# Kernel tuning notes

Hardware: AMD Instinct MI355X
Metric: run time of the kernel (lower is better)

The kernel has to match this reference:

```python
import jax, jax.numpy as jnp
import numpy as np

SIZE_DICT = 1024
DIM_DICT = 256
BETA = 0.001


def setup_inputs() -> dict:
    key = jax.random.key(0)
    k1, k2 = jax.random.split(key)
    z = jax.random.normal(k1, (64, 1024, DIM_DICT), dtype=jnp.float32)
    codebook = jax.random.normal(k2, (SIZE_DICT, DIM_DICT), dtype=jnp.float32)
    return {"z": z, "codebook": codebook, "flg_train": 1}


def reference(z, codebook, flg_train):
    zf = z.reshape(-1, DIM_DICT)  # [N, D]
    # squared euclidean distances: ||z||^2 + ||c||^2 - 2 z c^T  -> [N, K]
    d = (jnp.sum(zf ** 2, axis=1, keepdims=True)
         + jnp.sum(codebook ** 2, axis=1)
         - 2.0 * jnp.matmul(zf, codebook.T))
    idx = jnp.argmin(d, axis=1)  # [N]
    # one-hot @ codebook == gather
    z_q = codebook[idx].reshape(z.shape)
    if flg_train:
        loss = (jnp.mean((jax.lax.stop_gradient(z_q) - z) ** 2)
                + BETA * jnp.mean((z_q - jax.lax.stop_gradient(z)) ** 2))
    else:
        loss = jnp.float32(0.0)
    # straight-through estimator
    z_q = z + jax.lax.stop_gradient(z_q - z)
    # perplexity from codebook usage histogram (== mean of one-hot rows)
    n = zf.shape[0]
    counts = jax.ops.segment_sum(jnp.ones((n,), jnp.float32), idx,
                                 num_segments=SIZE_DICT)
    e_mean = counts / n
    perplexity = jnp.exp(-jnp.sum(e_mean * jnp.log(e_mean + 1e-10)))
    return (z_q, loss, perplexity)
```

## Files before the change

### kernel.cpp

```cpp
#include <hip/hip_runtime.h>


#define N_ROWS 65536
#define DIM    256
#define K_CODES 1024
#define BETA   0.001f

#define BM      128
#define NBLOCKS (N_ROWS / BM)
#define NTHREADS 512
#define CHUNK_BYTES 65536
#define NCHUNK  16

#define LO_SCALE 2048.0f
#define LO_INV   (1.0f / 2048.0f)

#define WS_BESTS_OFF 16384
#define WS_CBIMG_OFF 278528
#define WS_NEED (WS_CBIMG_OFF + NCHUNK * CHUNK_BYTES)

typedef _Float16 f16x8 __attribute__((ext_vector_type(8)));
typedef float f32x16 __attribute__((ext_vector_type(16)));


__global__ void cnorm_kernel(const float* __restrict__ cb, float* __restrict__ cnorm) {
    int k = blockIdx.x * blockDim.x + threadIdx.x;
    if (k >= K_CODES) return;
    const float4* row = (const float4*)(cb + (size_t)k * DIM);
    float s = 0.f;
#pragma unroll
    for (int j = 0; j < DIM / 4; ++j) {
        float4 v = row[j];
        s = fmaf(v.x, v.x, s);
        s = fmaf(v.y, v.y, s);
        s = fmaf(v.z, v.z, s);
        s = fmaf(v.w, v.w, s);
    }
    cnorm[k] = s;
}

__global__ void cb_prep(const float* __restrict__ cb, char* __restrict__ img) {
    int idx = blockIdx.x * blockDim.x + threadIdx.x;
    int c   = idx >> 5;
    int g32 = idx & 31;
    const float4* src = (const float4*)(cb + (size_t)c * DIM + g32 * 8);
    float4 v0 = src[0], v1 = src[1];
    float vv[8] = {v0.x, v0.y, v0.z, v0.w, v1.x, v1.y, v1.z, v1.w};
    f16x8 hi, lo;
#pragma unroll
    for (int j = 0; j < 8; ++j) {
        _Float16 h = (_Float16)vv[j];
        hi[j] = h;
        lo[j] = (_Float16)((vv[j] - (float)h) * LO_SCALE);
    }
    int kh = g32 >> 4;
    int gl = g32 & 15;
    int cl = c & 63;
    int unit = (c >> 6) * 2 + kh;
    size_t off = (size_t)unit * 32768 + (size_t)gl * 1024 + (size_t)cl * 16;
    *(f16x8*)(img + off) = hi;
    *(f16x8*)(img + off + 16384) = lo;
}


__device__ inline void stage_chunk(const char* img, int c, char* ldsbase, int tid) {
#pragma unroll
    for (int i = 0; i < 8; ++i) {
        __builtin_amdgcn_global_load_lds(
            (const __attribute__((address_space(1))) unsigned int*)
                (img + (size_t)c * CHUNK_BYTES + i * 8192 + tid * 16),
            (__attribute__((address_space(3))) unsigned int*)
                (ldsbase + i * 8192 + tid * 16),
            16, 0, 0);
    }
}

#define COMPUTE_CHUNK(BUF)                                                           \
    {                                                                                \
        const _Float16* bbase = csb + (BUF) * 32768 + crow * 8;                      \
        _Pragma("unroll")                                                            \
        for (int ks = 0; ks < 16; ++ks) {                                            \
            const _Float16* p = bbase + (ks >> 3) * 16384 + ((ks & 7) * 2 + lh) * 512;\
            f16x8 bh = *(const f16x8*)(p);                                           \
            f16x8 bl = *(const f16x8*)(p + 8192);                                    \
            f16x8 ah = zh[ks], al = zl[ks];                                          \
            acc_hh = __builtin_amdgcn_mfma_f32_32x32x16_f16(ah, bh, acc_hh, 0, 0, 0);\
            acc_x1 = __builtin_amdgcn_mfma_f32_32x32x16_f16(ah, bl, acc_x1, 0, 0, 0);\
            acc_x2 = __builtin_amdgcn_mfma_f32_32x32x16_f16(al, bh, acc_x2, 0, 0, 0);\
        }                                                                            \
    }

__global__ __launch_bounds__(NTHREADS, 2)
void vq_main_mfma(const float* __restrict__ z, const char* __restrict__ img,
                  const float* __restrict__ cnorm, int* __restrict__ bests_g,
                  int* __restrict__ counts, float* __restrict__ ploss) {
    __shared__ _Float16 csb[2 * 32768];
    __shared__ float bs2[BM][2];
    __shared__ int   bc2[BM][2];
    __shared__ float znorm_lds[BM];
    __shared__ float red[NTHREADS];

    const int tid  = threadIdx.x;
    const int lane = tid & 63;
    const int w    = tid >> 6;
    const int wr   = w >> 1;
    const int wc   = w & 1;
    const int l31  = lane & 31;
    const int lh   = lane >> 5;
    const int r0   = blockIdx.x * BM;

    stage_chunk(img, 0, (char*)csb, tid);

    const int zrow = wr * 32 + l31;
    f16x8 zh[16], zl[16];
    {
        const float* zr = z + (size_t)(r0 + zrow) * DIM;
        float zn = 0.f;
#pragma unroll
        for (int gi = 0; gi < 16; ++gi) {
            int g = gi * 2 + lh;
            float4 v0 = *(const float4*)(zr + g * 8);
            float4 v1 = *(const float4*)(zr + g * 8 + 4);
            float vv[8] = {v0.x, v0.y, v0.z, v0.w, v1.x, v1.y, v1.z, v1.w};
            f16x8 hi, lo;
#pragma unroll
            for (int j = 0; j < 8; ++j) {
                _Float16 h = (_Float16)vv[j];
                hi[j] = h;
                lo[j] = (_Float16)((vv[j] - (float)h) * LO_SCALE);
                zn = fmaf(vv[j], vv[j], zn);
            }
            zh[gi] = hi;
            zl[gi] = lo;
        }
        zn += __shfl_xor(zn, 32, 64);
        if (wc == 0 && lh == 0) znorm_lds[zrow] = zn;
    }

    f32x16 acc_hh, acc_x1, acc_x2;
#pragma unroll
    for (int e = 0; e < 16; ++e) { acc_hh[e] = 0.f; acc_x1[e] = 0.f; acc_x2[e] = 0.f; }
    float best_s[16];
    int   best_c[16];
#pragma unroll
    for (int e = 0; e < 16; ++e) { best_s[e] = 3.4e38f; best_c[e] = 0; }

    const int crow = wc * 32 + l31;

#pragma unroll 1
    for (int c = 0; c < NCHUNK; ++c) {
        const int b = c & 1;
        asm volatile("" ::: "memory");
        __builtin_amdgcn_s_barrier();
        asm volatile("" ::: "memory");
        if (c + 1 < NCHUNK) {
            stage_chunk(img, c + 1, (char*)csb + (b ^ 1) * CHUNK_BYTES, tid);
            asm volatile("s_waitcnt vmcnt(8)" ::: "memory");
        } else {
            asm volatile("s_waitcnt vmcnt(0)" ::: "memory");
        }
        __builtin_amdgcn_s_barrier();
        asm volatile("" ::: "memory");

        __builtin_amdgcn_s_setprio(1);
        COMPUTE_CHUNK(b)
        __builtin_amdgcn_s_setprio(0);

        {
            int col = c * 64 + crow;
            float cn = cnorm[col];
#pragma unroll
            for (int rg = 0; rg < 16; ++rg) {
                float dot = fmaf(acc_x1[rg] + acc_x2[rg], LO_INV, acc_hh[rg]);
                float s = fmaf(-2.0f, dot, cn);
                bool take = s < best_s[rg];
                best_s[rg] = take ? s : best_s[rg];
                best_c[rg] = take ? col : best_c[rg];
            }
#pragma unroll
            for (int e = 0; e < 16; ++e) { acc_hh[e] = 0.f; acc_x1[e] = 0.f; acc_x2[e] = 0.f; }
        }
    }

#pragma unroll
    for (int rg = 0; rg < 16; ++rg) {
        float bsv = best_s[rg];
        int   bcv = best_c[rg];
#pragma unroll
        for (int s = 1; s < 32; s <<= 1) {
            float os = __shfl_xor(bsv, s, 64);
            int   oc = __shfl_xor(bcv, s, 64);
            bool take = (os < bsv) || (os == bsv && oc < bcv);
            bsv = take ? os : bsv;
            bcv = take ? oc : bcv;
        }
        best_s[rg] = bsv;
        best_c[rg] = bcv;
    }
    if (l31 == 0) {
#pragma unroll
        for (int rg = 0; rg < 16; ++rg) {
            int rl = (rg & 3) + 8 * (rg >> 2) + 4 * lh;
            bs2[wr * 32 + rl][wc] = best_s[rg];
            bc2[wr * 32 + rl][wc] = best_c[rg];
        }
    }
    __syncthreads();

    float lsum = 0.f;
    if (tid < BM) {
        float s0 = bs2[tid][0], s1 = bs2[tid][1];
        int   c0 = bc2[tid][0], c1 = bc2[tid][1];
        bool t1 = (s1 < s0) || (s1 == s0 && c1 < c0);
        int   bc = t1 ? c1 : c0;
        float bs = t1 ? s1 : s0;
        bests_g[r0 + tid] = bc;
        atomicAdd(&counts[bc], 1);
        lsum = bs + znorm_lds[tid];
    }
    red[tid] = lsum;
    __syncthreads();
    for (int s = NTHREADS / 2; s > 0; s >>= 1) {
        if (tid < s) red[tid] += red[tid + s];
        __syncthreads();
    }
    if (tid == 0) ploss[blockIdx.x] = red[0];
}


__global__ __launch_bounds__(256)
void vq_gather(const float4* __restrict__ cb4, const int* __restrict__ bests,
               float4* __restrict__ out4) {
    int gid = blockIdx.x * blockDim.x + threadIdx.x;
    int row = gid >> 6;
    int q   = gid & 63;
    out4[gid] = cb4[(size_t)bests[row] * 64 + q];
}


#define FBM     32
#define FCHUNK  512
#define FDSTAGE 16
#define FCS_PAD 20
#define FNBLOCKS (N_ROWS / FBM)

__global__ __launch_bounds__(256, 2)
void vq_main_fp32(const float* __restrict__ z, const float* __restrict__ cb,
                  const float* __restrict__ cnorm, float* __restrict__ out,
                  int* __restrict__ counts, float* __restrict__ ploss) {
    __shared__ float zs[FBM][DIM];
    __shared__ float cs[FCHUNK][FCS_PAD];
    __shared__ int   bests[FBM];
    __shared__ float red[256];

    const int tid = threadIdx.x;
    const int tx  = tid & 63;
    const int ty  = tid >> 6;
    const int r0  = blockIdx.x * FBM;

    {
        const float4* zg  = (const float4*)(z + (size_t)r0 * DIM);
        float4*       zsv = (float4*)&zs[0][0];
#pragma unroll
        for (int j = 0; j < (FBM * DIM / 4) / 256; ++j)
            zsv[tid + 256 * j] = zg[tid + 256 * j];
    }

    unsigned long long best[8];
#pragma unroll
    for (int i = 0; i < 8; ++i) best[i] = ~0ull;

    for (int cb0 = 0; cb0 < K_CODES; cb0 += FCHUNK) {
        float acc[8][8];
#pragma unroll
        for (int i = 0; i < 8; ++i)
#pragma unroll
            for (int m = 0; m < 8; ++m) acc[i][m] = 0.f;

        for (int sd = 0; sd < DIM / FDSTAGE; ++sd) {
            __syncthreads();
#pragma unroll
            for (int j = 0; j < 8; ++j) {
                int f4i = tid + 256 * j;
                int c   = f4i >> 2;
                int qq  = f4i & 3;
                float4 v = *(const float4*)(cb + (size_t)(cb0 + c) * DIM + sd * FDSTAGE + qq * 4);
                *(float4*)&cs[c][qq * 4] = v;
            }
            __syncthreads();

#pragma unroll
            for (int dd4 = 0; dd4 < FDSTAGE / 4; ++dd4) {
                float4 zv[8], cv[8];
#pragma unroll
                for (int i = 0; i < 8; ++i)
                    zv[i] = *(const float4*)&zs[ty * 8 + i][sd * FDSTAGE + dd4 * 4];
#pragma unroll
                for (int m = 0; m < 8; ++m)
                    cv[m] = *(const float4*)&cs[tx + 64 * m][dd4 * 4];
#pragma unroll
                for (int i = 0; i < 8; ++i)
#pragma unroll
                    for (int m = 0; m < 8; ++m) {
                        float a = acc[i][m];
                        a = fmaf(zv[i].x, cv[m].x, a);
                        a = fmaf(zv[i].y, cv[m].y, a);
                        a = fmaf(zv[i].z, cv[m].z, a);
                        a = fmaf(zv[i].w, cv[m].w, a);
                        acc[i][m] = a;
                    }
            }
        }

#pragma unroll
        for (int m = 0; m < 8; ++m) {
            int   c  = cb0 + tx + 64 * m;
            float cn = cnorm[c];
#pragma unroll
            for (int i = 0; i < 8; ++i) {
                float s = fmaf(-2.f, acc[i][m], cn);
                unsigned u = __float_as_uint(s);
                u = (u & 0x80000000u) ? ~u : (u | 0x80000000u);
                unsigned long long key = ((unsigned long long)u << 32) | (unsigned)c;
                best[i] = key < best[i] ? key : best[i];
            }
        }
    }

#pragma unroll
    for (int i = 0; i < 8; ++i) {
        unsigned long long b = best[i];
#pragma unroll
        for (int s = 1; s < 64; s <<= 1) {
            unsigned long long o = __shfl_xor(b, s, 64);
            b = o < b ? o : b;
        }
        best[i] = b;
    }
    if (tx == 0)
#pragma unroll
        for (int i = 0; i < 8; ++i)
            bests[ty * 8 + i] = (int)(best[i] & 0xFFFFFFFFu);
    __syncthreads();

    const int r  = tid >> 3;
    const int lq = tid & 7;
    const int bidx = bests[r];
    const float4* crow = (const float4*)(cb + (size_t)bidx * DIM);
    const float4* zrow = (const float4*)&zs[r][0];
    float4*       orow = (float4*)(out + (size_t)(r0 + r) * DIM);
    float lsum = 0.f;
#pragma unroll
    for (int j = 0; j < 8; ++j) {
        int qg = lq + j * 8;
        float4 c4 = crow[qg];
        float4 z4 = zrow[qg];
        float4 o;
        float dx = c4.x - z4.x; o.x = z4.x + dx; lsum = fmaf(dx, dx, lsum);
        float dy = c4.y - z4.y; o.y = z4.y + dy; lsum = fmaf(dy, dy, lsum);
        float dz = c4.z - z4.z; o.z = z4.z + dz; lsum = fmaf(dz, dz, lsum);
        float dw = c4.w - z4.w; o.w = z4.w + dw; lsum = fmaf(dw, dw, lsum);
        orow[qg] = o;
    }
    if (tid < FBM) atomicAdd(&counts[bests[tid]], 1);

    red[tid] = lsum;
    __syncthreads();
    for (int s = 128; s > 0; s >>= 1) {
        if (tid < s) red[tid] += red[tid + s];
        __syncthreads();
    }
    if (tid == 0) ploss[blockIdx.x] = red[0];
}


__global__ void vq_final(const float* __restrict__ ploss, const int* __restrict__ counts,
                         const int* __restrict__ flg, float* __restrict__ out2, int np) {
    __shared__ float red[1024];
    const int t = threadIdx.x;

    float l = 0.f;
    for (int i = t; i < np; i += 1024) l += ploss[i];
    red[t] = l;
    __syncthreads();
    for (int s = 512; s > 0; s >>= 1) {
        if (t < s) red[t] += red[t + s];
        __syncthreads();
    }
    if (t == 0) {
        float loss = (red[0] / (float)((size_t)N_ROWS * DIM)) * (1.0f + BETA);
        if (flg[0] == 0) loss = 0.f;
        out2[0] = loss;
    }
    __syncthreads();

    float e = (float)counts[t] / (float)N_ROWS;
    red[t] = e * logf(e + 1e-10f);
    __syncthreads();
    for (int s = 512; s > 0; s >>= 1) {
        if (t < s) red[t] += red[t + s];
        __syncthreads();
    }
    if (t == 0) out2[1] = expf(-red[0]);
}

extern "C" void kernel_launch(void* const* d_in, const int* in_sizes, int n_in,
                              void* d_out, int out_size, void* d_ws, size_t ws_size,
                              hipStream_t stream) {
    const float* z   = (const float*)d_in[0];
    const float* cb  = (const float*)d_in[1];
    const int*   flg = (const int*)d_in[2];
    float* out = (float*)d_out;
    float* ws  = (float*)d_ws;

    float* cnorm  = ws;
    int*   counts = (int*)((char*)d_ws + 4096);
    float* ploss  = (float*)((char*)d_ws + 8192);
    int*   bests  = (int*)((char*)d_ws + WS_BESTS_OFF);
    char*  cbimg  = (char*)d_ws + WS_CBIMG_OFF;

    hipMemsetAsync(counts, 0, K_CODES * sizeof(int), stream);
    cnorm_kernel<<<K_CODES / 256, 256, 0, stream>>>(cb, cnorm);

    if (ws_size >= (size_t)WS_NEED) {
        cb_prep<<<128, 256, 0, stream>>>(cb, cbimg);
        vq_main_mfma<<<NBLOCKS, NTHREADS, 0, stream>>>(z, cbimg, cnorm, bests, counts, ploss);
        vq_gather<<<(N_ROWS * 64) / 256, 256, 0, stream>>>((const float4*)cb, bests, (float4*)out);
        vq_final<<<1, 1024, 0, stream>>>(ploss, counts, flg, out + (size_t)N_ROWS * DIM, NBLOCKS);
    } else {
        vq_main_fp32<<<FNBLOCKS, 256, 0, stream>>>(z, cb, cnorm, out, counts, ploss);
        vq_final<<<1, 1024, 0, stream>>>(ploss, counts, flg, out + (size_t)N_ROWS * DIM, FNBLOCKS);
    }
}
```

Measured before the change: 175.2 us.

## Stage codebook in half-K units to halve LDS double buffer

```diff
diff --git a/kernel.cpp b/kernel.cpp
--- a/kernel.cpp
+++ b/kernel.cpp
@@ -9,15 +9,15 @@
 #define BM      128
 #define NBLOCKS (N_ROWS / BM)
 #define NTHREADS 512
-#define CHUNK_BYTES 65536
-#define NCHUNK  16
+#define UNIT_BYTES 32768
+#define NUNIT   32
 
 #define LO_SCALE 2048.0f
 #define LO_INV   (1.0f / 2048.0f)
 
 #define WS_BESTS_OFF 16384
 #define WS_CBIMG_OFF 278528
-#define WS_NEED (WS_CBIMG_OFF + NCHUNK * CHUNK_BYTES)
+#define WS_NEED (WS_CBIMG_OFF + NUNIT * UNIT_BYTES)
 
 typedef _Float16 f16x8 __attribute__((ext_vector_type(8)));
 typedef float f32x16 __attribute__((ext_vector_type(16)));
@@ -57,33 +57,33 @@
     int gl = g32 & 15;
     int cl = c & 63;
     int unit = (c >> 6) * 2 + kh;
-    size_t off = (size_t)unit * 32768 + (size_t)gl * 1024 + (size_t)cl * 16;
+    size_t off = (size_t)unit * UNIT_BYTES + (size_t)gl * 1024 + (size_t)cl * 16;
     *(f16x8*)(img + off) = hi;
     *(f16x8*)(img + off + 16384) = lo;
 }
 
 
-__device__ inline void stage_chunk(const char* img, int c, char* ldsbase, int tid) {
-#pragma unroll
-    for (int i = 0; i < 8; ++i) {
+__device__ inline void stage_unit(const char* img, int u, char* ldsbase, int tid) {
+#pragma unroll
+    for (int i = 0; i < 4; ++i) {
         __builtin_amdgcn_global_load_lds(
             (const __attribute__((address_space(1))) unsigned int*)
-                (img + (size_t)c * CHUNK_BYTES + i * 8192 + tid * 16),
+                (img + (size_t)u * UNIT_BYTES + i * 8192 + tid * 16),
             (__attribute__((address_space(3))) unsigned int*)
                 (ldsbase + i * 8192 + tid * 16),
             16, 0, 0);
     }
 }
 
-#define COMPUTE_CHUNK(BUF)                                                           \
+#define COMPUTE_UNIT(KH, BUF)                                                        \
     {                                                                                \
-        const _Float16* bbase = csb + (BUF) * 32768 + crow * 8;                      \
+        const _Float16* bbase = csb + (BUF) * 16384 + crow * 8;                      \
         _Pragma("unroll")                                                            \
-        for (int ks = 0; ks < 16; ++ks) {                                            \
-            const _Float16* p = bbase + (ks >> 3) * 16384 + ((ks & 7) * 2 + lh) * 512;\
+        for (int ks = 0; ks < 8; ++ks) {                                             \
+            const _Float16* p = bbase + (ks * 2 + lh) * 512;                         \
             f16x8 bh = *(const f16x8*)(p);                                           \
             f16x8 bl = *(const f16x8*)(p + 8192);                                    \
-            f16x8 ah = zh[ks], al = zl[ks];                                          \
+            f16x8 ah = zh[(KH) * 8 + ks], al = zl[(KH) * 8 + ks];                    \
             acc_hh = __builtin_amdgcn_mfma_f32_32x32x16_f16(ah, bh, acc_hh, 0, 0, 0);\
             acc_x1 = __builtin_amdgcn_mfma_f32_32x32x16_f16(ah, bl, acc_x1, 0, 0, 0);\
             acc_x2 = __builtin_amdgcn_mfma_f32_32x32x16_f16(al, bh, acc_x2, 0, 0, 0);\
@@ -94,7 +94,7 @@
 void vq_main_mfma(const float* __restrict__ z, const char* __restrict__ img,
                   const float* __restrict__ cnorm, int* __restrict__ bests_g,
                   int* __restrict__ counts, float* __restrict__ ploss) {
-    __shared__ _Float16 csb[2 * 32768];
+    __shared__ _Float16 csb[2 * 16384];
     __shared__ float bs2[BM][2];
     __shared__ int   bc2[BM][2];
     __shared__ float znorm_lds[BM];
@@ -109,7 +109,7 @@
     const int lh   = lane >> 5;
     const int r0   = blockIdx.x * BM;
 
-    stage_chunk(img, 0, (char*)csb, tid);
+    stage_unit(img, 0, (char*)csb, tid);
 
     const int zrow = wr * 32 + l31;
     f16x8 zh[16], zl[16];
@@ -148,26 +148,27 @@
     const int crow = wc * 32 + l31;
 
 #pragma unroll 1
-    for (int c = 0; c < NCHUNK; ++c) {
-        const int b = c & 1;
+    for (int u = 0; u < NUNIT; ++u) {
+        const int b = u & 1;
         asm volatile("" ::: "memory");
         __builtin_amdgcn_s_barrier();
         asm volatile("" ::: "memory");
-        if (c + 1 < NCHUNK) {
-            stage_chunk(img, c + 1, (char*)csb + (b ^ 1) * CHUNK_BYTES, tid);
-            asm volatile("s_waitcnt vmcnt(8)" ::: "memory");
+        if (u + 1 < NUNIT) {
+            stage_unit(img, u + 1, (char*)csb + (b ^ 1) * UNIT_BYTES, tid);
+            asm volatile("s_waitcnt vmcnt(4)" ::: "memory");
         } else {
             asm volatile("s_waitcnt vmcnt(0)" ::: "memory");
         }
         __builtin_amdgcn_s_barrier();
         asm volatile("" ::: "memory");
 
+        const int kh = u & 1;
         __builtin_amdgcn_s_setprio(1);
-        COMPUTE_CHUNK(b)
+        if (kh == 0) { COMPUTE_UNIT(0, b) } else { COMPUTE_UNIT(1, b) }
         __builtin_amdgcn_s_setprio(0);
 
-        {
-            int col = c * 64 + crow;
+        if (kh == 1) {
+            int col = (u >> 1) * 64 + crow;
             float cn = cnorm[col];
 #pragma unroll
             for (int rg = 0; rg < 16; ++rg) {
```

New measurement: 202.3 us. 15.5% more time.

## Split chunk compute into four phases interleaving LDS loads, MFMA and barriers

Applied to the files above, without the earlier changes.

```diff
diff --git a/kernel.cpp b/kernel.cpp
--- a/kernel.cpp
+++ b/kernel.cpp
@@ -75,19 +75,44 @@
     }
 }
 
-#define COMPUTE_CHUNK(BUF)                                                           \
+#define LOADB(KS, BH, BL)                                                            \
     {                                                                                \
-        const _Float16* bbase = csb + (BUF) * 32768 + crow * 8;                      \
-        _Pragma("unroll")                                                            \
-        for (int ks = 0; ks < 16; ++ks) {                                            \
-            const _Float16* p = bbase + (ks >> 3) * 16384 + ((ks & 7) * 2 + lh) * 512;\
-            f16x8 bh = *(const f16x8*)(p);                                           \
-            f16x8 bl = *(const f16x8*)(p + 8192);                                    \
-            f16x8 ah = zh[ks], al = zl[ks];                                          \
-            acc_hh = __builtin_amdgcn_mfma_f32_32x32x16_f16(ah, bh, acc_hh, 0, 0, 0);\
-            acc_x1 = __builtin_amdgcn_mfma_f32_32x32x16_f16(ah, bl, acc_x1, 0, 0, 0);\
-            acc_x2 = __builtin_amdgcn_mfma_f32_32x32x16_f16(al, bh, acc_x2, 0, 0, 0);\
-        }                                                                            \
+        const _Float16* p = bbase + ((KS) >> 3) * 16384 + (((KS) & 7) * 2 + lh) * 512;\
+        BH = *(const f16x8*)(p);                                                     \
+        BL = *(const f16x8*)(p + 8192);                                              \
+    }
+
+#define MF3(KS, BH, BL)                                                              \
+    {                                                                                \
+        f16x8 ah = zh[KS], al = zl[KS];                                              \
+        acc_hh = __builtin_amdgcn_mfma_f32_32x32x16_f16(ah, BH, acc_hh, 0, 0, 0);    \
+        acc_x1 = __builtin_amdgcn_mfma_f32_32x32x16_f16(ah, BL, acc_x1, 0, 0, 0);    \
+        acc_x2 = __builtin_amdgcn_mfma_f32_32x32x16_f16(al, BH, acc_x2, 0, 0, 0);    \
+    }
+
+#define PHASE(P)                                                                     \
+    {                                                                                \
+        f16x8 bh0, bl0, bh1, bl1, bh2, bl2, bh3, bl3;                                \
+        LOADB((P) * 4 + 0, bh0, bl0)                                                 \
+        LOADB((P) * 4 + 1, bh1, bl1)                                                 \
+        LOADB((P) * 4 + 2, bh2, bl2)                                                 \
+        LOADB((P) * 4 + 3, bh3, bl3)                                                 \
+        if ((P) == 0 && c + 1 < NCHUNK)                                              \
+            stage_chunk(img, c + 1, (char*)csb + (b ^ 1) * CHUNK_BYTES, tid);        \
+        asm volatile("" ::: "memory");                                               \
+        __builtin_amdgcn_s_barrier();                                                \
+        asm volatile("" ::: "memory");                                               \
+        __builtin_amdgcn_s_setprio(1);                                               \
+        MF3((P) * 4 + 0, bh0, bl0)                                                   \
+        MF3((P) * 4 + 1, bh1, bl1)                                                   \
+        MF3((P) * 4 + 2, bh2, bl2)                                                   \
+        MF3((P) * 4 + 3, bh3, bl3)                                                   \
+        __builtin_amdgcn_s_setprio(0);                                               \
+        if ((P) == 3)                                                                \
+            asm volatile("s_waitcnt vmcnt(0)" ::: "memory");                         \
+        asm volatile("" ::: "memory");                                               \
+        __builtin_amdgcn_s_barrier();                                                \
+        asm volatile("" ::: "memory");                                               \
     }
 
 __global__ __launch_bounds__(NTHREADS, 2)
@@ -137,6 +162,10 @@
         if (wc == 0 && lh == 0) znorm_lds[zrow] = zn;
     }
 
+    asm volatile("s_waitcnt vmcnt(0)" ::: "memory");
+    __builtin_amdgcn_s_barrier();
+    asm volatile("" ::: "memory");
+
     f32x16 acc_hh, acc_x1, acc_x2;
 #pragma unroll
     for (int e = 0; e < 16; ++e) { acc_hh[e] = 0.f; acc_x1[e] = 0.f; acc_x2[e] = 0.f; }
@@ -150,25 +179,16 @@
 #pragma unroll 1
     for (int c = 0; c < NCHUNK; ++c) {
         const int b = c & 1;
-        asm volatile("" ::: "memory");
-        __builtin_amdgcn_s_barrier();
-        asm volatile("" ::: "memory");
-        if (c + 1 < NCHUNK) {
-            stage_chunk(img, c + 1, (char*)csb + (b ^ 1) * CHUNK_BYTES, tid);
-            asm volatile("s_waitcnt vmcnt(8)" ::: "memory");
-        } else {
-            asm volatile("s_waitcnt vmcnt(0)" ::: "memory");
-        }
-        __builtin_amdgcn_s_barrier();
-        asm volatile("" ::: "memory");
-
-        __builtin_amdgcn_s_setprio(1);
-        COMPUTE_CHUNK(b)
-        __builtin_amdgcn_s_setprio(0);
+        const _Float16* bbase = csb + b * 32768 + crow * 8;
+        float cn = cnorm[c * 64 + crow];
+
+        PHASE(0)
+        PHASE(1)
+        PHASE(2)
+        PHASE(3)
 
         {
             int col = c * 64 + crow;
-            float cn = cnorm[col];
 #pragma unroll
             for (int rg = 0; rg < 16; ++rg) {
                 float dot = fmaf(acc_x1[rg] + acc_x2[rg], LO_INV, acc_hh[rg]);
```

Result: no change. 176.8 us (+0.9%).
